# Optimization experiments

Hardware: AMD Instinct MI355X
Metric: run time of the kernel (lower is better)

## Reference

```python
import jax, jax.numpy as jnp
import numpy as np

H = 16  # hidden_state_size

def setup_inputs() -> dict:
    key = jax.random.key(0)
    k = jax.random.split(key, 6)
    E, DE = 1600000, 32
    return {
        "h": jax.random.normal(k[0], (E, H), dtype=jnp.float32),
        "e": jax.random.normal(k[1], (E, DE), dtype=jnp.float32),
        "W1": jax.random.normal(k[2], (DE, H * H), dtype=jnp.float32) * 0.05,
        "b1": jax.random.normal(k[3], (H * H,), dtype=jnp.float32) * 0.05,
        "W2": jax.random.normal(k[4], (DE, H), dtype=jnp.float32) * 0.05,
        "b2": jax.random.normal(k[5], (H,), dtype=jnp.float32) * 0.05,
    }

def reference(h, e, W1, b1, W2, b2):
    E = e.shape[0]
    # dense1: [E, H*H] -> reshape to per-edge matrix [E, H, H]
    A = (e @ W1 + b1).reshape(E, H, H)
    # batched matvec: m_ei = sum_j A[e,i,j] * h[e,j]
    m = jnp.einsum('eij,ej->ei', A, h)
    # dense2 bias term
    b = e @ W2 + b2
    return m + b
```

## Files before the change

### kernel.cpp

```cpp
#include <hip/hip_runtime.h>
#include <hip/hip_bf16.h>


using f16x8  = __attribute__((ext_vector_type(8))) _Float16;
using f16x2  = __attribute__((ext_vector_type(2))) _Float16;
using fp16v2 = __attribute__((ext_vector_type(2))) __fp16;
using f32x4  = __attribute__((ext_vector_type(4))) float;
using u32x4  = __attribute__((ext_vector_type(4))) unsigned int;

static __device__ __forceinline__ unsigned int pkrtz(float lo, float hi) {
    fp16v2 p = __builtin_amdgcn_cvt_pkrtz(lo, hi);
    return __builtin_bit_cast(unsigned int, p);
}
static __device__ __forceinline__ f16x2 u2h(unsigned int u) {
    return __builtin_bit_cast(f16x2, u);
}
static __device__ __forceinline__ unsigned int h2u(f16x2 h) {
    return __builtin_bit_cast(unsigned int, h);
}
static __device__ __forceinline__ unsigned short f2h_bits(float x) {
    _Float16 h = (_Float16)x;
    return __builtin_bit_cast(unsigned short, h);
}
static __device__ __forceinline__ unsigned int bperm(int baddr, unsigned int src) {
    return (unsigned int)__builtin_amdgcn_ds_bpermute(baddr, (int)src);
}

__global__ void __launch_bounds__(256) msg_kernel(
    const float* __restrict__ hptr, const float* __restrict__ eptr,
    const float* __restrict__ W1,   const float* __restrict__ b1,
    const float* __restrict__ W2,   const float* __restrict__ b2,
    float* __restrict__ out, int E)
{
    __shared__ __align__(16) unsigned short Bs[18 * 64 * 8];

    const int lane = threadIdx.x & 63;
    const int g    = lane >> 4;
    const int r    = lane & 15;
    const int wv   = threadIdx.x >> 6;

    #pragma unroll
    for (int tq = 0; tq < 2; ++tq) {
        const int t = wv * 2 + tq;
        const int d = g * 8 + t;
        const float4* wp = (const float4*)(W1 + (size_t)d * 256 + r * 16);
        const float4 w0 = wp[0], w1 = wp[1], w2 = wp[2], w3 = wp[3];
        Bs[( 0*64 + lane)*8 + t] = f2h_bits(w0.x);
        Bs[( 1*64 + lane)*8 + t] = f2h_bits(w0.y);
        Bs[( 2*64 + lane)*8 + t] = f2h_bits(w0.z);
        Bs[( 3*64 + lane)*8 + t] = f2h_bits(w0.w);
        Bs[( 4*64 + lane)*8 + t] = f2h_bits(w1.x);
        Bs[( 5*64 + lane)*8 + t] = f2h_bits(w1.y);
        Bs[( 6*64 + lane)*8 + t] = f2h_bits(w1.z);
        Bs[( 7*64 + lane)*8 + t] = f2h_bits(w1.w);
        Bs[( 8*64 + lane)*8 + t] = f2h_bits(w2.x);
        Bs[( 9*64 + lane)*8 + t] = f2h_bits(w2.y);
        Bs[(10*64 + lane)*8 + t] = f2h_bits(w2.z);
        Bs[(11*64 + lane)*8 + t] = f2h_bits(w2.w);
        Bs[(12*64 + lane)*8 + t] = f2h_bits(w3.x);
        Bs[(13*64 + lane)*8 + t] = f2h_bits(w3.y);
        Bs[(14*64 + lane)*8 + t] = f2h_bits(w3.z);
        Bs[(15*64 + lane)*8 + t] = f2h_bits(w3.w);
        Bs[(16*64 + lane)*8 + t] = f2h_bits(W2[d * 16 + r]);
        float v;
        if (d < 16)       v = b1[r * 16 + d];
        else if (d == 16) v = b2[r];
        else              v = 0.0f;
        Bs[(17*64 + lane)*8 + t] = f2h_bits(v);
    }
    __syncthreads();

    const int ntiles = (E + 15) >> 4;
    const int nwaves = (gridDim.x * blockDim.x) >> 6;
    const int wid    = (blockIdx.x * blockDim.x + threadIdx.x) >> 6;
    if (wid >= ntiles) return;

    const unsigned short* bsl = &Bs[lane * 8];

    const int ba0 = (r      ) << 2;
    const int ba1 = (r + 16 ) << 2;
    const int ba2 = (r + 32 ) << 2;
    const int ba3 = (r + 48 ) << 2;

#define LDSB(KK) __builtin_bit_cast(f16x8, *reinterpret_cast<const u32x4*>(bsl + (KK) * 512))

#define LOADT(T, E0, E1, H0) { \
        int tt = (T); if (tt >= ntiles) tt = ntiles - 1; \
        int cc = tt * 16 + r; if (cc >= E) cc = E - 1; \
        const float4* ep_ = (const float4*)(eptr + (size_t)cc * 32 + g * 8); \
        E0 = ep_[0]; E1 = ep_[1]; \
        H0 = *(const float4*)(hptr + (size_t)cc * 16 + g * 4); }

#define MB(HPQ, HALF, BF, ACC) { \
        const f16x2 hv_ = u2h(HPQ); \
        const f16x2 hh_ = {hv_[HALF], hv_[HALF]}; \
        u32x4 u_ = {h2u(hh_ * u2h(eP0)), h2u(hh_ * u2h(eP1)), \
                    h2u(hh_ * u2h(eP2)), h2u(hh_ * u2h(eP3))}; \
        ACC = __builtin_amdgcn_mfma_f32_16x16x32_f16( \
            __builtin_bit_cast(f16x8, u_), BF, ACC, 0, 0, 0); }

    float4 sE0, sE1, sH;
    int t = wid;
    LOADT(t, sE0, sE1, sH);

    while (true) {
        f16x8 Fb0 = LDSB(0), Fb1 = LDSB(1);

        const unsigned int eP0 = pkrtz(sE0.x, sE0.y), eP1 = pkrtz(sE0.z, sE0.w);
        const unsigned int eP2 = pkrtz(sE1.x, sE1.y), eP3 = pkrtz(sE1.z, sE1.w);
        const unsigned int hQ0 = pkrtz(sH.x, sH.y),   hQ1 = pkrtz(sH.z, sH.w);

        LOADT(t + nwaves, sE0, sE1, sH);

        const unsigned int hP0 = bperm(ba0, hQ0), hP1 = bperm(ba0, hQ1);
        const unsigned int hP2 = bperm(ba1, hQ0), hP3 = bperm(ba1, hQ1);
        const unsigned int hP4 = bperm(ba2, hQ0), hP5 = bperm(ba2, hQ1);
        const unsigned int hP6 = bperm(ba3, hQ0), hP7 = bperm(ba3, hQ1);

        f32x4 acc0 = {0.0f, 0.0f, 0.0f, 0.0f};
        f32x4 acc1 = {0.0f, 0.0f, 0.0f, 0.0f};

        MB(hP0, 0, Fb0, acc0)  Fb0 = LDSB( 2);
        MB(hP0, 1, Fb1, acc1)  Fb1 = LDSB( 3);
        MB(hP1, 0, Fb0, acc0)  Fb0 = LDSB( 4);
        MB(hP1, 1, Fb1, acc1)  Fb1 = LDSB( 5);
        MB(hP2, 0, Fb0, acc0)  Fb0 = LDSB( 6);
        MB(hP2, 1, Fb1, acc1)  Fb1 = LDSB( 7);
        MB(hP3, 0, Fb0, acc0)  Fb0 = LDSB( 8);
        MB(hP3, 1, Fb1, acc1)  Fb1 = LDSB( 9);
        MB(hP4, 0, Fb0, acc0)  Fb0 = LDSB(10);
        MB(hP4, 1, Fb1, acc1)  Fb1 = LDSB(11);
        MB(hP5, 0, Fb0, acc0)  Fb0 = LDSB(12);
        MB(hP5, 1, Fb1, acc1)  Fb1 = LDSB(13);
        MB(hP6, 0, Fb0, acc0)  Fb0 = LDSB(14);
        MB(hP6, 1, Fb1, acc1)  Fb1 = LDSB(15);
        MB(hP7, 0, Fb0, acc0)  Fb0 = LDSB(16);
        MB(hP7, 1, Fb1, acc1)  Fb1 = LDSB(17);

        {
            u32x4 u_ = {eP0, eP1, eP2, eP3};
            acc0 = __builtin_amdgcn_mfma_f32_16x16x32_f16(
                __builtin_bit_cast(f16x8, u_), Fb0, acc0, 0, 0, 0);
        }
        {
            const unsigned int a0 = (g == 0) ? hP0 : (g == 1) ? hP4
                                   : (g == 2) ? 0x00003C00u : 0u;
            const unsigned int a1 = (g == 0) ? hP1 : (g == 1) ? hP5 : 0u;
            const unsigned int a2 = (g == 0) ? hP2 : (g == 1) ? hP6 : 0u;
            const unsigned int a3 = (g == 0) ? hP3 : (g == 1) ? hP7 : 0u;
            u32x4 u_ = {a0, a1, a2, a3};
            acc1 = __builtin_amdgcn_mfma_f32_16x16x32_f16(
                __builtin_bit_cast(f16x8, u_), Fb1, acc1, 0, 0, 0);
        }

        const int rowbase = t * 16 + g * 4;
        float* op = out + (size_t)rowbase * 16 + r;
        const float s0 = acc0[0] + acc1[0], s1 = acc0[1] + acc1[1];
        const float s2 = acc0[2] + acc1[2], s3 = acc0[3] + acc1[3];
        if (rowbase + 3 < E) { op[0] = s0; op[16] = s1; op[32] = s2; op[48] = s3; }
        else {
            if (rowbase     < E) op[ 0] = s0;
            if (rowbase + 1 < E) op[16] = s1;
            if (rowbase + 2 < E) op[32] = s2;
        }

        t += nwaves;
        if (t >= ntiles) break;
    }

#undef MB
#undef LOADT
#undef LDSB
}

extern "C" void kernel_launch(void* const* d_in, const int* in_sizes, int n_in,
                              void* d_out, int out_size, void* d_ws, size_t ws_size,
                              hipStream_t stream) {
    const float* h  = (const float*)d_in[0];
    const float* e  = (const float*)d_in[1];
    const float* W1 = (const float*)d_in[2];
    const float* b1 = (const float*)d_in[3];
    const float* W2 = (const float*)d_in[4];
    const float* b2 = (const float*)d_in[5];
    float* out = (float*)d_out;

    const int E = in_sizes[0] / 16;

    dim3 grid(2048), block(256);
    hipLaunchKernelGGL(msg_kernel, grid, block, 0, stream,
                       h, e, W1, b1, W2, b2, out, E);
}
```

Before: 85.28 us.

## Prefetch edge and hidden tiles via async global-to-LDS double-buffered ring

Replaces the register-held one-tile-ahead prefetch of e and h with global_load_lds transfers into a per-wave two-slot LDS ring. Each wave keeps two tiles in flight and waits with an explicit vmcnt before reading the current slot from LDS. The goal is more memory-level parallelism and lower register pressure in this bandwidth-bound kernel. The cost is about 24 KB of extra LDS per block, which may reduce occupancy, plus an extra LDS round trip and hand-placed waitcnts that also end up waiting on earlier stores.

```diff
diff --git a/kernel.cpp b/kernel.cpp
--- a/kernel.cpp
+++ b/kernel.cpp
@@ -33,6 +33,7 @@
     float* __restrict__ out, int E)
 {
     __shared__ __align__(16) unsigned short Bs[18 * 64 * 8];
+    __shared__ __align__(16) char ring[4 * 2 * 3072];
 
     const int lane = threadIdx.x & 63;
     const int g    = lane >> 4;
@@ -82,14 +83,24 @@
     const int ba2 = (r + 32 ) << 2;
     const int ba3 = (r + 48 ) << 2;
 
+    __attribute__((address_space(3))) char* rw =
+        (__attribute__((address_space(3))) char*)ring + wv * 6144;
+    const char* rr = ring + wv * 6144;
+
 #define LDSB(KK) __builtin_bit_cast(f16x8, *reinterpret_cast<const u32x4*>(bsl + (KK) * 512))
 
-#define LOADT(T, E0, E1, H0) { \
+#define GLL(GP, LP) __builtin_amdgcn_global_load_lds( \
+        (const __attribute__((address_space(1))) void*)(GP), \
+        (__attribute__((address_space(3))) void*)(LP), 16, 0, 0)
+
+#define ISSUE(T, SLOT) { \
         int tt = (T); if (tt >= ntiles) tt = ntiles - 1; \
         int cc = tt * 16 + r; if (cc >= E) cc = E - 1; \
-        const float4* ep_ = (const float4*)(eptr + (size_t)cc * 32 + g * 8); \
-        E0 = ep_[0]; E1 = ep_[1]; \
-        H0 = *(const float4*)(hptr + (size_t)cc * 16 + g * 4); }
+        const float* ge_ = eptr + (size_t)cc * 32 + g * 8; \
+        const float* gh_ = hptr + (size_t)cc * 16 + g * 4; \
+        GLL(ge_,     rw + (SLOT) * 3072       ); \
+        GLL(ge_ + 4, rw + (SLOT) * 3072 + 1024); \
+        GLL(gh_,     rw + (SLOT) * 3072 + 2048); }
 
 #define MB(HPQ, HALF, BF, ACC) { \
         const f16x2 hv_ = u2h(HPQ); \
@@ -99,18 +110,24 @@
         ACC = __builtin_amdgcn_mfma_f32_16x16x32_f16( \
             __builtin_bit_cast(f16x8, u_), BF, ACC, 0, 0, 0); }
 
-    float4 sE0, sE1, sH;
     int t = wid;
-    LOADT(t, sE0, sE1, sH);
+    ISSUE(t, 0);
+    ISSUE(t + nwaves, 1);
+    int slot = 0;
 
     while (true) {
+        asm volatile("s_waitcnt vmcnt(3)" ::: "memory");
+
+        const char* lb = rr + slot * 3072 + lane * 16;
+        const float4 E0 = *(const float4*)(lb);
+        const float4 E1 = *(const float4*)(lb + 1024);
+        const float4 Hq = *(const float4*)(lb + 2048);
+
         f16x8 Fb0 = LDSB(0), Fb1 = LDSB(1);
 
-        const unsigned int eP0 = pkrtz(sE0.x, sE0.y), eP1 = pkrtz(sE0.z, sE0.w);
-        const unsigned int eP2 = pkrtz(sE1.x, sE1.y), eP3 = pkrtz(sE1.z, sE1.w);
-        const unsigned int hQ0 = pkrtz(sH.x, sH.y),   hQ1 = pkrtz(sH.z, sH.w);
-
-        LOADT(t + nwaves, sE0, sE1, sH);
+        const unsigned int eP0 = pkrtz(E0.x, E0.y), eP1 = pkrtz(E0.z, E0.w);
+        const unsigned int eP2 = pkrtz(E1.x, E1.y), eP3 = pkrtz(E1.z, E1.w);
+        const unsigned int hQ0 = pkrtz(Hq.x, Hq.y), hQ1 = pkrtz(Hq.z, Hq.w);
 
         const unsigned int hP0 = bperm(ba0, hQ0), hP1 = bperm(ba0, hQ1);
         const unsigned int hP2 = bperm(ba1, hQ0), hP3 = bperm(ba1, hQ1);
@@ -164,12 +181,17 @@
             if (rowbase + 2 < E) op[32] = s2;
         }
 
+        asm volatile("s_waitcnt lgkmcnt(0)" ::: "memory");
+        ISSUE(t + 2 * nwaves, slot);
+
+        slot ^= 1;
         t += nwaves;
         if (t >= ntiles) break;
     }
 
 #undef MB
-#undef LOADT
+#undef ISSUE
+#undef GLL
 #undef LDSB
 }
 
```

Measured after the change: 90.58 us. 6.2% more time.

## Process two edge tiles per wave iteration sharing LDS weight fragments

Applied to the files above, without the earlier changes.

Each wave now handles a pair of 16-edge tiles per loop iteration. Every W1/W2 fragment read from LDS is used by two MFMAs, one per tile, which halves LDS reads per tile and gives the scheduler more independent MFMA chains. The bpermute calls move inline, next to where each fragment block is used, and output writes become nontemporal stores. The cost is higher register pressure from doubled prefetch buffers and accumulators, and fewer work units per wave.

```diff
diff --git a/kernel.cpp b/kernel.cpp
--- a/kernel.cpp
+++ b/kernel.cpp
@@ -71,9 +71,10 @@
     __syncthreads();
 
     const int ntiles = (E + 15) >> 4;
+    const int npairs = (ntiles + 1) >> 1;
     const int nwaves = (gridDim.x * blockDim.x) >> 6;
     const int wid    = (blockIdx.x * blockDim.x + threadIdx.x) >> 6;
-    if (wid >= ntiles) return;
+    if (wid >= npairs) return;
 
     const unsigned short* bsl = &Bs[lane * 8];
 
@@ -84,92 +85,133 @@
 
 #define LDSB(KK) __builtin_bit_cast(f16x8, *reinterpret_cast<const u32x4*>(bsl + (KK) * 512))
 
-#define LOADT(T, E0, E1, H0) { \
-        int tt = (T); if (tt >= ntiles) tt = ntiles - 1; \
-        int cc = tt * 16 + r; if (cc >= E) cc = E - 1; \
-        const float4* ep_ = (const float4*)(eptr + (size_t)cc * 32 + g * 8); \
-        E0 = ep_[0]; E1 = ep_[1]; \
-        H0 = *(const float4*)(hptr + (size_t)cc * 16 + g * 4); }
-
-#define MB(HPQ, HALF, BF, ACC) { \
+#define LOADP(P, AE0, AE1, AH, BE0, BE1, BH) { \
+        int pp = (P); if (pp >= npairs) pp = npairs - 1; \
+        int t1_ = pp * 2 + 1; if (t1_ >= ntiles) t1_ = ntiles - 1; \
+        int c0_ = pp * 2 * 16 + r; if (c0_ >= E) c0_ = E - 1; \
+        int c1_ = t1_ * 16 + r;    if (c1_ >= E) c1_ = E - 1; \
+        const float4* eA_ = (const float4*)(eptr + (size_t)c0_ * 32 + g * 8); \
+        AE0 = eA_[0]; AE1 = eA_[1]; \
+        AH  = *(const float4*)(hptr + (size_t)c0_ * 16 + g * 4); \
+        const float4* eB_ = (const float4*)(eptr + (size_t)c1_ * 32 + g * 8); \
+        BE0 = eB_[0]; BE1 = eB_[1]; \
+        BH  = *(const float4*)(hptr + (size_t)c1_ * 16 + g * 4); }
+
+#define MB(HPQ, HALF, FB, ACC, EP0, EP1, EP2, EP3) { \
         const f16x2 hv_ = u2h(HPQ); \
         const f16x2 hh_ = {hv_[HALF], hv_[HALF]}; \
-        u32x4 u_ = {h2u(hh_ * u2h(eP0)), h2u(hh_ * u2h(eP1)), \
-                    h2u(hh_ * u2h(eP2)), h2u(hh_ * u2h(eP3))}; \
+        u32x4 u_ = {h2u(hh_ * u2h(EP0)), h2u(hh_ * u2h(EP1)), \
+                    h2u(hh_ * u2h(EP2)), h2u(hh_ * u2h(EP3))}; \
         ACC = __builtin_amdgcn_mfma_f32_16x16x32_f16( \
-            __builtin_bit_cast(f16x8, u_), BF, ACC, 0, 0, 0); }
-
-    float4 sE0, sE1, sH;
-    int t = wid;
-    LOADT(t, sE0, sE1, sH);
+            __builtin_bit_cast(f16x8, u_), FB, ACC, 0, 0, 0); }
+
+#define QBLK(BA, K0) { \
+        const unsigned int hALo = bperm(BA, hQA0), hAHi = bperm(BA, hQA1); \
+        const unsigned int hBLo = bperm(BA, hQB0), hBHi = bperm(BA, hQB1); \
+        f16x8 Fb_; \
+        Fb_ = LDSB(K0    ); MB(hALo, 0, Fb_, accA0, eAP0,eAP1,eAP2,eAP3) \
+                            MB(hBLo, 0, Fb_, accB0, eBP0,eBP1,eBP2,eBP3) \
+        Fb_ = LDSB(K0 + 1); MB(hALo, 1, Fb_, accA1, eAP0,eAP1,eAP2,eAP3) \
+                            MB(hBLo, 1, Fb_, accB1, eBP0,eBP1,eBP2,eBP3) \
+        Fb_ = LDSB(K0 + 2); MB(hAHi, 0, Fb_, accA0, eAP0,eAP1,eAP2,eAP3) \
+                            MB(hBHi, 0, Fb_, accB0, eBP0,eBP1,eBP2,eBP3) \
+        Fb_ = LDSB(K0 + 3); MB(hAHi, 1, Fb_, accA1, eAP0,eAP1,eAP2,eAP3) \
+                            MB(hBHi, 1, Fb_, accB1, eBP0,eBP1,eBP2,eBP3) }
+
+    float4 aE0, aE1, aH, bE0, bE1, bH;
+    int p = wid;
+    LOADP(p, aE0, aE1, aH, bE0, bE1, bH);
 
     while (true) {
-        f16x8 Fb0 = LDSB(0), Fb1 = LDSB(1);
-
-        const unsigned int eP0 = pkrtz(sE0.x, sE0.y), eP1 = pkrtz(sE0.z, sE0.w);
-        const unsigned int eP2 = pkrtz(sE1.x, sE1.y), eP3 = pkrtz(sE1.z, sE1.w);
-        const unsigned int hQ0 = pkrtz(sH.x, sH.y),   hQ1 = pkrtz(sH.z, sH.w);
-
-        LOADT(t + nwaves, sE0, sE1, sH);
-
-        const unsigned int hP0 = bperm(ba0, hQ0), hP1 = bperm(ba0, hQ1);
-        const unsigned int hP2 = bperm(ba1, hQ0), hP3 = bperm(ba1, hQ1);
-        const unsigned int hP4 = bperm(ba2, hQ0), hP5 = bperm(ba2, hQ1);
-        const unsigned int hP6 = bperm(ba3, hQ0), hP7 = bperm(ba3, hQ1);
-
-        f32x4 acc0 = {0.0f, 0.0f, 0.0f, 0.0f};
-        f32x4 acc1 = {0.0f, 0.0f, 0.0f, 0.0f};
-
-        MB(hP0, 0, Fb0, acc0)  Fb0 = LDSB( 2);
-        MB(hP0, 1, Fb1, acc1)  Fb1 = LDSB( 3);
-        MB(hP1, 0, Fb0, acc0)  Fb0 = LDSB( 4);
-        MB(hP1, 1, Fb1, acc1)  Fb1 = LDSB( 5);
-        MB(hP2, 0, Fb0, acc0)  Fb0 = LDSB( 6);
-        MB(hP2, 1, Fb1, acc1)  Fb1 = LDSB( 7);
-        MB(hP3, 0, Fb0, acc0)  Fb0 = LDSB( 8);
-        MB(hP3, 1, Fb1, acc1)  Fb1 = LDSB( 9);
-        MB(hP4, 0, Fb0, acc0)  Fb0 = LDSB(10);
-        MB(hP4, 1, Fb1, acc1)  Fb1 = LDSB(11);
-        MB(hP5, 0, Fb0, acc0)  Fb0 = LDSB(12);
-        MB(hP5, 1, Fb1, acc1)  Fb1 = LDSB(13);
-        MB(hP6, 0, Fb0, acc0)  Fb0 = LDSB(14);
-        MB(hP6, 1, Fb1, acc1)  Fb1 = LDSB(15);
-        MB(hP7, 0, Fb0, acc0)  Fb0 = LDSB(16);
-        MB(hP7, 1, Fb1, acc1)  Fb1 = LDSB(17);
+        const unsigned int eAP0 = pkrtz(aE0.x, aE0.y), eAP1 = pkrtz(aE0.z, aE0.w);
+        const unsigned int eAP2 = pkrtz(aE1.x, aE1.y), eAP3 = pkrtz(aE1.z, aE1.w);
+        const unsigned int hQA0 = pkrtz(aH.x, aH.y),   hQA1 = pkrtz(aH.z, aH.w);
+        const unsigned int eBP0 = pkrtz(bE0.x, bE0.y), eBP1 = pkrtz(bE0.z, bE0.w);
+        const unsigned int eBP2 = pkrtz(bE1.x, bE1.y), eBP3 = pkrtz(bE1.z, bE1.w);
+        const unsigned int hQB0 = pkrtz(bH.x, bH.y),   hQB1 = pkrtz(bH.z, bH.w);
+
+        LOADP(p + nwaves, aE0, aE1, aH, bE0, bE1, bH);
+
+        f32x4 accA0 = {0.0f, 0.0f, 0.0f, 0.0f};
+        f32x4 accA1 = {0.0f, 0.0f, 0.0f, 0.0f};
+        f32x4 accB0 = {0.0f, 0.0f, 0.0f, 0.0f};
+        f32x4 accB1 = {0.0f, 0.0f, 0.0f, 0.0f};
+
+        QBLK(ba0,  0)
+        QBLK(ba1,  4)
+        QBLK(ba2,  8)
+        QBLK(ba3, 12)
 
         {
-            u32x4 u_ = {eP0, eP1, eP2, eP3};
-            acc0 = __builtin_amdgcn_mfma_f32_16x16x32_f16(
-                __builtin_bit_cast(f16x8, u_), Fb0, acc0, 0, 0, 0);
+            const f16x8 Fb_ = LDSB(16);
+            u32x4 uA_ = {eAP0, eAP1, eAP2, eAP3};
+            accA0 = __builtin_amdgcn_mfma_f32_16x16x32_f16(
+                __builtin_bit_cast(f16x8, uA_), Fb_, accA0, 0, 0, 0);
+            u32x4 uB_ = {eBP0, eBP1, eBP2, eBP3};
+            accB0 = __builtin_amdgcn_mfma_f32_16x16x32_f16(
+                __builtin_bit_cast(f16x8, uB_), Fb_, accB0, 0, 0, 0);
         }
         {
-            const unsigned int a0 = (g == 0) ? hP0 : (g == 1) ? hP4
-                                   : (g == 2) ? 0x00003C00u : 0u;
-            const unsigned int a1 = (g == 0) ? hP1 : (g == 1) ? hP5 : 0u;
-            const unsigned int a2 = (g == 0) ? hP2 : (g == 1) ? hP6 : 0u;
-            const unsigned int a3 = (g == 0) ? hP3 : (g == 1) ? hP7 : 0u;
-            u32x4 u_ = {a0, a1, a2, a3};
-            acc1 = __builtin_amdgcn_mfma_f32_16x16x32_f16(
-                __builtin_bit_cast(f16x8, u_), Fb1, acc1, 0, 0, 0);
+            const int bx0 = (g == 1) ? ba2 : ba0;
+            const int bx1 = (g == 1) ? ba3 : ba1;
+            unsigned int aA0 = bperm(bx0, hQA0), aA1 = bperm(bx0, hQA1);
+            unsigned int aA2 = bperm(bx1, hQA0), aA3 = bperm(bx1, hQA1);
+            unsigned int aB0 = bperm(bx0, hQB0), aB1 = bperm(bx0, hQB1);
+            unsigned int aB2 = bperm(bx1, hQB0), aB3 = bperm(bx1, hQB1);
+            if (g >= 2) {
+                const unsigned int one = (g == 2) ? 0x00003C00u : 0u;
+                aA0 = one; aA1 = 0u; aA2 = 0u; aA3 = 0u;
+                aB0 = one; aB1 = 0u; aB2 = 0u; aB3 = 0u;
+            }
+            const f16x8 Fb_ = LDSB(17);
+            u32x4 uA_ = {aA0, aA1, aA2, aA3};
+            accA1 = __builtin_amdgcn_mfma_f32_16x16x32_f16(
+                __builtin_bit_cast(f16x8, uA_), Fb_, accA1, 0, 0, 0);
+            u32x4 uB_ = {aB0, aB1, aB2, aB3};
+            accB1 = __builtin_amdgcn_mfma_f32_16x16x32_f16(
+                __builtin_bit_cast(f16x8, uB_), Fb_, accB1, 0, 0, 0);
         }
 
-        const int rowbase = t * 16 + g * 4;
-        float* op = out + (size_t)rowbase * 16 + r;
-        const float s0 = acc0[0] + acc1[0], s1 = acc0[1] + acc1[1];
-        const float s2 = acc0[2] + acc1[2], s3 = acc0[3] + acc1[3];
-        if (rowbase + 3 < E) { op[0] = s0; op[16] = s1; op[32] = s2; op[48] = s3; }
-        else {
-            if (rowbase     < E) op[ 0] = s0;
-            if (rowbase + 1 < E) op[16] = s1;
-            if (rowbase + 2 < E) op[32] = s2;
+        {
+            const int t0s = p * 2;
+            int t1s = t0s + 1; if (t1s >= ntiles) t1s = ntiles - 1;
+            const int rbA = t0s * 16 + g * 4;
+            float* opA = out + (size_t)rbA * 16 + r;
+            const float sA0 = accA0[0] + accA1[0], sA1 = accA0[1] + accA1[1];
+            const float sA2 = accA0[2] + accA1[2], sA3 = accA0[3] + accA1[3];
+            if (rbA + 3 < E) {
+                __builtin_nontemporal_store(sA0, opA);
+                __builtin_nontemporal_store(sA1, opA + 16);
+                __builtin_nontemporal_store(sA2, opA + 32);
+                __builtin_nontemporal_store(sA3, opA + 48);
+            } else {
+                if (rbA     < E) __builtin_nontemporal_store(sA0, opA);
+                if (rbA + 1 < E) __builtin_nontemporal_store(sA1, opA + 16);
+                if (rbA + 2 < E) __builtin_nontemporal_store(sA2, opA + 32);
+            }
+            const int rbB = t1s * 16 + g * 4;
+            float* opB = out + (size_t)rbB * 16 + r;
+            const float sB0 = accB0[0] + accB1[0], sB1 = accB0[1] + accB1[1];
+            const float sB2 = accB0[2] + accB1[2], sB3 = accB0[3] + accB1[3];
+            if (rbB + 3 < E) {
+                __builtin_nontemporal_store(sB0, opB);
+                __builtin_nontemporal_store(sB1, opB + 16);
+                __builtin_nontemporal_store(sB2, opB + 32);
+                __builtin_nontemporal_store(sB3, opB + 48);
+            } else {
+                if (rbB     < E) __builtin_nontemporal_store(sB0, opB);
+                if (rbB + 1 < E) __builtin_nontemporal_store(sB1, opB + 16);
+                if (rbB + 2 < E) __builtin_nontemporal_store(sB2, opB + 32);
+            }
         }
 
-        t += nwaves;
-        if (t >= ntiles) break;
+        p += nwaves;
+        if (p >= npairs) break;
     }
 
+#undef QBLK
 #undef MB
-#undef LOADT
+#undef LOADP
 #undef LDSB
 }
 
```

New measurement: 77.76 us. 1.1x faster.
